# Kernel optimization log

Hardware: AMD Instinct MI355X
Metric: run time of the kernel (lower is better)

Reference implementation:

```python
import jax, jax.numpy as jnp
import numpy as np

N_NODES = 50000
N_EDGES = 640000
D_IN = 128
D_H = 128


def gcn_conv(x, edge_index_sl, W, b, n_nodes):
    # x: [N, d_in]; edge_index_sl: [2, E+N] (self-loops already appended)
    h = x @ W  # [N, d_out]
    row, col = edge_index_sl[0], edge_index_sl[1]
    deg = jax.ops.segment_sum(jnp.ones(row.shape[0], dtype=x.dtype), col,
                              num_segments=n_nodes)
    dis = jnp.where(deg > 0, jax.lax.rsqrt(jnp.maximum(deg, 1e-12)), 0.0)
    norm = dis[row] * dis[col]  # [E+N]
    msg = h[row] * norm[:, None]  # gather + scale, [E+N, d_out]
    out = jax.ops.segment_sum(msg, col, num_segments=n_nodes)  # scatter-add
    return out + b


def setup_inputs() -> dict:
    key = jax.random.key(0)
    ks = jax.random.split(key, 9)
    x = jax.random.normal(ks[0], (N_NODES, D_IN), dtype=jnp.float32)
    edge_index = jax.random.randint(ks[1], (2, N_EDGES), 0, N_NODES, dtype=jnp.int64)
    s0 = 1.0 / np.sqrt(D_IN)
    s1 = 1.0 / np.sqrt(D_H)
    W0 = jax.random.uniform(ks[2], (D_IN, D_H), jnp.float32, -s0, s0)
    b0 = jnp.zeros((D_H,), jnp.float32)
    W1 = jax.random.uniform(ks[3], (D_H, D_H), jnp.float32, -s1, s1)
    b1 = jnp.zeros((D_H,), jnp.float32)
    W2 = jax.random.uniform(ks[4], (D_H, D_H), jnp.float32, -s1, s1)
    b2 = jnp.zeros((D_H,), jnp.float32)
    return {"x": x, "edge_index": edge_index, "W0": W0, "b0": b0,
            "W1": W1, "b1": b1, "W2": W2, "b2": b2}


def reference(x, edge_index, W0, b0, W1, b1, W2, b2):
    n = x.shape[0]
    # GCNConv adds self-loops: append (i, i) for every node.
    loops = jnp.arange(n, dtype=edge_index.dtype)
    ei = jnp.concatenate([edge_index, jnp.stack([loops, loops])], axis=1)
    h = x
    for W, b in ((W0, b0), (W1, b1), (W2, b2)):
        h = gcn_conv(h, ei, W, b, n)
        h = jax.nn.relu(h)  # dropout is identity in eval mode
    return h
```

## Files before the change

### kernel.cpp

```cpp
#include <hip/hip_runtime.h>
#include <hip/hip_bf16.h>

#define D 128
#define CAP 64
typedef _Float16 f16;
typedef unsigned short u16;
typedef f16 f16x8 __attribute__((ext_vector_type(8)));
typedef f16 f16x4 __attribute__((ext_vector_type(4)));
typedef float f32x4 __attribute__((ext_vector_type(4)));



__global__ void scatter_cvt_kernel(const int* __restrict__ row, const int* __restrict__ col,
                                   int* __restrict__ fill, u16* __restrict__ ssrc, int E,
                                   const float* __restrict__ W0, const float* __restrict__ W1,
                                   const float* __restrict__ W2,
                                   const float* __restrict__ b0, const float* __restrict__ b1,
                                   const float* __restrict__ b2,
                                   f16* __restrict__ WT, float* __restrict__ bperm) {
    const int EB = (E + 255) >> 8;
    const int b = blockIdx.x;
    if (b < EB) {
        int i = b * 256 + threadIdx.x;
        if (i < E) {
            int d = col[i];
            int p = atomicAdd(&fill[d], 1);
            if (p < CAP) ssrc[(size_t)d * CAP + p] = (u16)row[i];
        }
    } else {
        int id = (b - EB) * 256 + threadIdx.x;
        if (id < 49152) {
            int l = id >> 14;
            int e = id & 16383;
            int j = e >> 7;
            int nn = e & 127;
            int k = (l == 0) ? j : ((j >> 3) + 16 * (j & 7));
            const float* W = (l == 0) ? W0 : (l == 1) ? W1 : W2;
            WT[(size_t)l * 16384 + nn * 128 + j] = (f16)W[k * 128 + nn];
        } else if (id < 49536) {
            int j = id - 49152;
            int l = j >> 7;
            int pos = j & 127;
            int c = 16 * (pos & 7) + (pos >> 3);
            const float* bb = (l == 0) ? b0 : (l == 1) ? b1 : b2;
            bperm[l * 128 + pos] = bb[c];
        }
    }
}


template <bool A_F32>
__global__ __launch_bounds__(256) void gemm_mfma(const void* __restrict__ Aptr,
                                                 const f16* __restrict__ WT,
                                                 const int* __restrict__ fill,
                                                 f16* __restrict__ H, int n) {
    __shared__ f16 sW[128 * 128];
    const int tid  = threadIdx.x;
    const int w    = tid >> 6, lane = tid & 63;
    const int q    = lane >> 4, c = lane & 15;
    const int row0 = blockIdx.x * 64;

    int arow = row0 + w * 16 + c;
    if (arow >= n) arow = n - 1;

    f16x8 afr[4];
    if (A_F32) {
        float4 x0[4], x1[4];
        #pragma unroll
        for (int t = 0; t < 4; ++t) {
            const float* src = (const float*)Aptr + (size_t)arow * D + (t * 4 + q) * 8;
            x0[t] = *(const float4*)src;
            x1[t] = *(const float4*)(src + 4);
        }
        #pragma unroll
        for (int t = 0; t < 4; ++t) {
            f16x8 h;
            h[0] = (f16)x0[t].x; h[1] = (f16)x0[t].y; h[2] = (f16)x0[t].z; h[3] = (f16)x0[t].w;
            h[4] = (f16)x1[t].x; h[5] = (f16)x1[t].y; h[6] = (f16)x1[t].z; h[7] = (f16)x1[t].w;
            afr[t] = h;
        }
    } else {
        #pragma unroll
        for (int t = 0; t < 4; ++t)
            afr[t] = *(const f16x8*)((const f16*)Aptr + (size_t)arow * D + (t * 4 + q) * 8);
    }

    #pragma unroll
    for (int i = 0; i < 8; ++i) {
        int f = i * 256 + tid;
        int r = f >> 4, b = f & 15;
        int u = (r << 4) | (b ^ (r & 15));
        *(f16x8*)&sW[u * 8] = *(const f16x8*)&WT[(size_t)r * D + b * 8];
    }
    __syncthreads();

    f32x4 acc[8];
    #pragma unroll
    for (int nt = 0; nt < 8; ++nt) acc[nt] = (f32x4)0.f;

    #pragma unroll
    for (int nt = 0; nt < 8; ++nt) {
        const int rn = nt * 16 + c;
        #pragma unroll
        for (int t = 0; t < 4; ++t) {
            f16x8 bfr = *(const f16x8*)&sW[(((rn << 4) | ((t * 4 + q) ^ c))) * 8];
            acc[nt] = __builtin_amdgcn_mfma_f32_16x16x32_f16(afr[t], bfr, acc[nt], 0, 0, 0);
        }
    }

    const int rbase = row0 + w * 16 + q * 4;
    int4 fv4 = *(const int4*)&fill[rbase];
    #pragma unroll
    for (int reg = 0; reg < 4; ++reg) {
        int grow = rbase + reg;
        if (grow < n) {
            int fv = (reg == 0) ? fv4.x : (reg == 1) ? fv4.y : (reg == 2) ? fv4.z : fv4.w;
            float dv = rsqrtf((float)(fv + 1));
            f16x8 hh;
            #pragma unroll
            for (int nt = 0; nt < 8; ++nt) hh[nt] = (f16)(acc[nt][reg] * dv);
            *(f16x8*)&H[(size_t)grow * D + c * 8] = hh;
        } else {
            const f16x8 z = {};
            *(f16x8*)&H[(size_t)grow * D + c * 8] = z;
        }
    }
}


template <bool LAST>
__global__ __launch_bounds__(256) void agg_kernel(const f16* __restrict__ H,
                                                  const int* __restrict__ fill,
                                                  const u16* __restrict__ ssrc,
                                                  const float* __restrict__ bperm,
                                                  float* __restrict__ out,
                                                  f16* __restrict__ act, int n) {
    const int tid  = threadIdx.x;
    const int wid  = (blockIdx.x << 2) | (tid >> 6);
    const int half = (tid >> 5) & 1;
    const int l    = tid & 31;
    int v = wid * 2 + half;
    const bool valid = (v < n);
    if (!valid) v = n - 1;
    const int fo = l * 4;
    const int zr = n;

    const u16* sp = &ssrc[(size_t)v * CAP];

    int4 sv0 = *(const int4*)sp;
    int4 sv1 = *(const int4*)(sp + 8);
    f16x4 hv = *(const f16x4*)&H[(size_t)v * D + fo];
    const int truedeg = fill[v];

    int deg = truedeg > CAP ? CAP : truedeg;
    int nb  = (deg + 15) >> 4;
    int nbo = __shfl_xor(nb, 32);
    const int nbmax = nb > nbo ? nb : nbo;

    float a0 = (float)hv[0], a1 = (float)hv[1], a2 = (float)hv[2], a3 = (float)hv[3];

    for (int b = 0; b < nbmax; ++b) {
        const int4 c0 = sv0, c1 = sv1;
        if (b + 1 < nbmax) {
            sv0 = *(const int4*)(sp + (b + 1) * 16);
            sv1 = *(const int4*)(sp + (b + 1) * 16 + 8);
        }
        const int rem = deg - b * 16;
        const int wv[8] = {c0.x, c0.y, c0.z, c0.w, c1.x, c1.y, c1.z, c1.w};
        f16x4 g[16];
        #pragma unroll
        for (int j = 0; j < 16; ++j) {
            int iv = (wv[j >> 1] >> ((j & 1) * 16)) & 0xffff;
            iv = (j < rem) ? iv : zr;
            g[j] = *(const f16x4*)&H[(size_t)iv * D + fo];
        }
        #pragma unroll
        for (int j = 0; j < 16; j += 4) {
            a0 += ((float)g[j][0] + (float)g[j + 1][0]) + ((float)g[j + 2][0] + (float)g[j + 3][0]);
            a1 += ((float)g[j][1] + (float)g[j + 1][1]) + ((float)g[j + 2][1] + (float)g[j + 3][1]);
            a2 += ((float)g[j][2] + (float)g[j + 1][2]) + ((float)g[j + 2][2] + (float)g[j + 3][2]);
            a3 += ((float)g[j][3] + (float)g[j + 1][3]) + ((float)g[j + 2][3] + (float)g[j + 3][3]);
        }
    }

    const float dv = rsqrtf((float)(truedeg + 1));
    const float4 bb = *(const float4*)&bperm[fo];
    float r0 = fmaxf(fmaf(dv, a0, bb.x), 0.f);
    float r1 = fmaxf(fmaf(dv, a1, bb.y), 0.f);
    float r2 = fmaxf(fmaf(dv, a2, bb.z), 0.f);
    float r3 = fmaxf(fmaf(dv, a3, bb.w), 0.f);

    if (valid) {
        if (LAST) {
            const int cb = (l & 1) * 64 + (l >> 1);
            float* op = out + (size_t)v * D + cb;
            op[0]  = r0;
            op[16] = r1;
            op[32] = r2;
            op[48] = r3;
        } else {
            f16x4 res;
            res[0] = (f16)r0; res[1] = (f16)r1; res[2] = (f16)r2; res[3] = (f16)r3;
            *(f16x4*)&act[(size_t)v * D + fo] = res;
        }
    }
}


extern "C" void kernel_launch(void* const* d_in, const int* in_sizes, int n_in,
                              void* d_out, int out_size, void* d_ws, size_t ws_size,
                              hipStream_t stream) {
    const float* x  = (const float*)d_in[0];
    const int*   ei = (const int*)d_in[1];
    const float* W0 = (const float*)d_in[2];
    const float* b0 = (const float*)d_in[3];
    const float* W1 = (const float*)d_in[4];
    const float* b1 = (const float*)d_in[5];
    const float* W2 = (const float*)d_in[6];
    const float* b2 = (const float*)d_in[7];
    float* out = (float*)d_out;

    const int n = in_sizes[0] / D;
    const int E = in_sizes[1] / 2;
    const int n_pad = (n + 64) & ~63;
    const int* row = ei;
    const int* col = ei + E;
    const int EB = (E + 255) / 256;

    char* w = (char*)d_ws;
    size_t o = 0;
    f16* hbuf = (f16*)(w + o); o += (size_t)n_pad * D * 2;
    f16* act  = (f16*)(w + o); o += (size_t)n_pad * D * 2;
    f16* WT   = (f16*)(w + o); o += (size_t)3 * 16384 * 2;
    o = (o + 63) & ~(size_t)63;
    float* bperm = (float*)(w + o); o += 3 * 128 * 4;
    int* fill = (int*)(w + o); o += (size_t)n_pad * 4;
    o = (o + 127) & ~(size_t)127;
    u16* ssrc = (u16*)(w + o);

    hipMemsetAsync(fill, 0, (size_t)n_pad * 4, stream);
    scatter_cvt_kernel<<<EB + 194, 256, 0, stream>>>(row, col, fill, ssrc, E,
                                                     W0, W1, W2, b0, b1, b2, WT, bperm);

    const int gblocks = n_pad >> 6;
    const int aggwaves = (n + 1) >> 1;
    const int ablocks = (aggwaves + 3) >> 2;

    gemm_mfma<true><<<gblocks, 256, 0, stream>>>(x, WT, fill, hbuf, n);
    agg_kernel<false><<<ablocks, 256, 0, stream>>>(hbuf, fill, ssrc, bperm, out, act, n);
    gemm_mfma<false><<<gblocks, 256, 0, stream>>>(act, WT + 16384, fill, hbuf, n);
    agg_kernel<false><<<ablocks, 256, 0, stream>>>(hbuf, fill, ssrc, bperm + 128, out, act, n);
    gemm_mfma<false><<<gblocks, 256, 0, stream>>>(act, WT + 2 * 16384, fill, hbuf, n);
    agg_kernel<true><<<ablocks, 256, 0, stream>>>(hbuf, fill, ssrc, bperm + 256, out, act, n);
}
```

Measured before the change: 235.3 us.

## Fuse aggregation with next layer's GEMM via shared-memory activation tile

The layer-1 and layer-2 aggregations are merged with the following layer's MFMA GEMM into one kernel. Each wave aggregates 16 rows into a swizzled LDS tile, then feeds that tile directly as the A fragment. This removes the f16 activation round trip through global memory and two kernel launches, and ping-pongs between two H buffers. In exchange each block reloads the 32KB weight tile and uses more LDS, which lowers occupancy for the latency-bound gather phase. Each wave also processes 8 node pairs serially, giving less parallelism per wave than the standalone aggregation kernel.

```diff
diff --git a/kernel.cpp b/kernel.cpp
--- a/kernel.cpp
+++ b/kernel.cpp
@@ -49,8 +49,7 @@
 }
 
 
-template <bool A_F32>
-__global__ __launch_bounds__(256) void gemm_mfma(const void* __restrict__ Aptr,
+__global__ __launch_bounds__(256) void gemm_mfma(const float* __restrict__ Aptr,
                                                  const f16* __restrict__ WT,
                                                  const int* __restrict__ fill,
                                                  f16* __restrict__ H, int n) {
@@ -64,11 +63,11 @@
     if (arow >= n) arow = n - 1;
 
     f16x8 afr[4];
-    if (A_F32) {
+    {
         float4 x0[4], x1[4];
         #pragma unroll
         for (int t = 0; t < 4; ++t) {
-            const float* src = (const float*)Aptr + (size_t)arow * D + (t * 4 + q) * 8;
+            const float* src = Aptr + (size_t)arow * D + (t * 4 + q) * 8;
             x0[t] = *(const float4*)src;
             x1[t] = *(const float4*)(src + 4);
         }
@@ -79,10 +78,6 @@
             h[4] = (f16)x1[t].x; h[5] = (f16)x1[t].y; h[6] = (f16)x1[t].z; h[7] = (f16)x1[t].w;
             afr[t] = h;
         }
-    } else {
-        #pragma unroll
-        for (int t = 0; t < 4; ++t)
-            afr[t] = *(const f16x8*)((const f16*)Aptr + (size_t)arow * D + (t * 4 + q) * 8);
     }
 
     #pragma unroll
@@ -128,13 +123,129 @@
 }
 
 
-template <bool LAST>
-__global__ __launch_bounds__(256) void agg_kernel(const f16* __restrict__ H,
-                                                  const int* __restrict__ fill,
-                                                  const u16* __restrict__ ssrc,
-                                                  const float* __restrict__ bperm,
-                                                  float* __restrict__ out,
-                                                  f16* __restrict__ act, int n) {
+__global__ __launch_bounds__(256) void fused_agg_gemm(const f16* __restrict__ Hin,
+                                                      const int* __restrict__ fill,
+                                                      const u16* __restrict__ ssrc,
+                                                      const float* __restrict__ bperm,
+                                                      const f16* __restrict__ WT,
+                                                      f16* __restrict__ Hout, int n) {
+    __shared__ f16 sW[128 * 128];
+    __shared__ f16 sA[4][16 * 128];
+    const int tid  = threadIdx.x;
+    const int w    = tid >> 6, lane = tid & 63;
+    const int q    = lane >> 4, c = lane & 15;
+    const int row0 = blockIdx.x * 64;
+
+    #pragma unroll
+    for (int i = 0; i < 8; ++i) {
+        int f = i * 256 + tid;
+        int r = f >> 4, b = f & 15;
+        int u = (r << 4) | (b ^ (r & 15));
+        *(f16x8*)&sW[u * 8] = *(const f16x8*)&WT[(size_t)r * D + b * 8];
+    }
+    __syncthreads();
+
+    const int h32 = (lane >> 5) & 1;
+    const int l   = lane & 31;
+    const int fo  = l * 4;
+    const int zr  = n;
+    const float4 bb = *(const float4*)&bperm[fo];
+
+    for (int p = 0; p < 8; ++p) {
+        int v = row0 + w * 16 + p * 2 + h32;
+        int vc = (v < n) ? v : (n - 1);
+        const u16* sp = &ssrc[(size_t)vc * CAP];
+        int4 sv0 = *(const int4*)sp;
+        int4 sv1 = *(const int4*)(sp + 8);
+        f16x4 hv = *(const f16x4*)&Hin[(size_t)vc * D + fo];
+        const int truedeg = fill[vc];
+
+        int deg = truedeg > CAP ? CAP : truedeg;
+        int nb  = (deg + 15) >> 4;
+        int nbo = __shfl_xor(nb, 32);
+        const int nbmax = nb > nbo ? nb : nbo;
+
+        float a0 = (float)hv[0], a1 = (float)hv[1], a2 = (float)hv[2], a3 = (float)hv[3];
+
+        for (int b = 0; b < nbmax; ++b) {
+            const int4 c0 = sv0, c1 = sv1;
+            if (b + 1 < nbmax) {
+                sv0 = *(const int4*)(sp + (b + 1) * 16);
+                sv1 = *(const int4*)(sp + (b + 1) * 16 + 8);
+            }
+            const int rem = deg - b * 16;
+            const int wv[8] = {c0.x, c0.y, c0.z, c0.w, c1.x, c1.y, c1.z, c1.w};
+            f16x4 g[16];
+            #pragma unroll
+            for (int j = 0; j < 16; ++j) {
+                int iv = (wv[j >> 1] >> ((j & 1) * 16)) & 0xffff;
+                iv = (j < rem) ? iv : zr;
+                g[j] = *(const f16x4*)&Hin[(size_t)iv * D + fo];
+            }
+            #pragma unroll
+            for (int j = 0; j < 16; j += 4) {
+                a0 += ((float)g[j][0] + (float)g[j+1][0]) + ((float)g[j+2][0] + (float)g[j+3][0]);
+                a1 += ((float)g[j][1] + (float)g[j+1][1]) + ((float)g[j+2][1] + (float)g[j+3][1]);
+                a2 += ((float)g[j][2] + (float)g[j+1][2]) + ((float)g[j+2][2] + (float)g[j+3][2]);
+                a3 += ((float)g[j][3] + (float)g[j+1][3]) + ((float)g[j+2][3] + (float)g[j+3][3]);
+            }
+        }
+
+        const float dv = rsqrtf((float)(truedeg + 1));
+        f16x4 res;
+        res[0] = (f16)fmaxf(fmaf(dv, a0, bb.x), 0.f);
+        res[1] = (f16)fmaxf(fmaf(dv, a1, bb.y), 0.f);
+        res[2] = (f16)fmaxf(fmaf(dv, a2, bb.z), 0.f);
+        res[3] = (f16)fmaxf(fmaf(dv, a3, bb.w), 0.f);
+
+        const int rL = p * 2 + h32;
+        *(f16x4*)&sA[w][((((rL << 4) | ((l >> 1) ^ (rL & 15)))) << 3) + (l & 1) * 4] = res;
+    }
+
+    f16x8 afr[4];
+    #pragma unroll
+    for (int t = 0; t < 4; ++t)
+        afr[t] = *(const f16x8*)&sA[w][(((c << 4) | ((t * 4 + q) ^ (c & 15)))) << 3];
+
+    f32x4 acc[8];
+    #pragma unroll
+    for (int nt = 0; nt < 8; ++nt) acc[nt] = (f32x4)0.f;
+
+    #pragma unroll
+    for (int nt = 0; nt < 8; ++nt) {
+        const int rn = nt * 16 + c;
+        #pragma unroll
+        for (int t = 0; t < 4; ++t) {
+            f16x8 bfr = *(const f16x8*)&sW[(((rn << 4) | ((t * 4 + q) ^ c))) * 8];
+            acc[nt] = __builtin_amdgcn_mfma_f32_16x16x32_f16(afr[t], bfr, acc[nt], 0, 0, 0);
+        }
+    }
+
+    const int rbase = row0 + w * 16 + q * 4;
+    int4 fv4 = *(const int4*)&fill[rbase];
+    #pragma unroll
+    for (int reg = 0; reg < 4; ++reg) {
+        int grow = rbase + reg;
+        if (grow < n) {
+            int fv = (reg == 0) ? fv4.x : (reg == 1) ? fv4.y : (reg == 2) ? fv4.z : fv4.w;
+            float dv = rsqrtf((float)(fv + 1));
+            f16x8 hh;
+            #pragma unroll
+            for (int nt = 0; nt < 8; ++nt) hh[nt] = (f16)(acc[nt][reg] * dv);
+            *(f16x8*)&Hout[(size_t)grow * D + c * 8] = hh;
+        } else {
+            const f16x8 z = {};
+            *(f16x8*)&Hout[(size_t)grow * D + c * 8] = z;
+        }
+    }
+}
+
+
+__global__ __launch_bounds__(256) void agg_last(const f16* __restrict__ H,
+                                                const int* __restrict__ fill,
+                                                const u16* __restrict__ ssrc,
+                                                const float* __restrict__ bperm,
+                                                float* __restrict__ out, int n) {
     const int tid  = threadIdx.x;
     const int wid  = (blockIdx.x << 2) | (tid >> 6);
     const int half = (tid >> 5) & 1;
@@ -146,7 +257,6 @@
     const int zr = n;
 
     const u16* sp = &ssrc[(size_t)v * CAP];
-
     int4 sv0 = *(const int4*)sp;
     int4 sv1 = *(const int4*)(sp + 8);
     f16x4 hv = *(const f16x4*)&H[(size_t)v * D + fo];
@@ -176,10 +286,10 @@
         }
         #pragma unroll
         for (int j = 0; j < 16; j += 4) {
-            a0 += ((float)g[j][0] + (float)g[j + 1][0]) + ((float)g[j + 2][0] + (float)g[j + 3][0]);
-            a1 += ((float)g[j][1] + (float)g[j + 1][1]) + ((float)g[j + 2][1] + (float)g[j + 3][1]);
-            a2 += ((float)g[j][2] + (float)g[j + 1][2]) + ((float)g[j + 2][2] + (float)g[j + 3][2]);
-            a3 += ((float)g[j][3] + (float)g[j + 1][3]) + ((float)g[j + 2][3] + (float)g[j + 3][3]);
+            a0 += ((float)g[j][0] + (float)g[j+1][0]) + ((float)g[j+2][0] + (float)g[j+3][0]);
+            a1 += ((float)g[j][1] + (float)g[j+1][1]) + ((float)g[j+2][1] + (float)g[j+3][1]);
+            a2 += ((float)g[j][2] + (float)g[j+1][2]) + ((float)g[j+2][2] + (float)g[j+3][2]);
+            a3 += ((float)g[j][3] + (float)g[j+1][3]) + ((float)g[j+2][3] + (float)g[j+3][3]);
         }
     }
 
@@ -191,18 +301,12 @@
     float r3 = fmaxf(fmaf(dv, a3, bb.w), 0.f);
 
     if (valid) {
-        if (LAST) {
-            const int cb = (l & 1) * 64 + (l >> 1);
-            float* op = out + (size_t)v * D + cb;
-            op[0]  = r0;
-            op[16] = r1;
-            op[32] = r2;
-            op[48] = r3;
-        } else {
-            f16x4 res;
-            res[0] = (f16)r0; res[1] = (f16)r1; res[2] = (f16)r2; res[3] = (f16)r3;
-            *(f16x4*)&act[(size_t)v * D + fo] = res;
-        }
+        const int cb = (l & 1) * 64 + (l >> 1);
+        float* op = out + (size_t)v * D + cb;
+        op[0]  = r0;
+        op[16] = r1;
+        op[32] = r2;
+        op[48] = r3;
     }
 }
 
@@ -229,9 +333,9 @@
 
     char* w = (char*)d_ws;
     size_t o = 0;
-    f16* hbuf = (f16*)(w + o); o += (size_t)n_pad * D * 2;
-    f16* act  = (f16*)(w + o); o += (size_t)n_pad * D * 2;
-    f16* WT   = (f16*)(w + o); o += (size_t)3 * 16384 * 2;
+    f16* hbufA = (f16*)(w + o); o += (size_t)n_pad * D * 2;
+    f16* hbufB = (f16*)(w + o); o += (size_t)n_pad * D * 2;
+    f16* WT    = (f16*)(w + o); o += (size_t)3 * 16384 * 2;
     o = (o + 63) & ~(size_t)63;
     float* bperm = (float*)(w + o); o += 3 * 128 * 4;
     int* fill = (int*)(w + o); o += (size_t)n_pad * 4;
@@ -246,10 +350,10 @@
     const int aggwaves = (n + 1) >> 1;
     const int ablocks = (aggwaves + 3) >> 2;
 
-    gemm_mfma<true><<<gblocks, 256, 0, stream>>>(x, WT, fill, hbuf, n);
-    agg_kernel<false><<<ablocks, 256, 0, stream>>>(hbuf, fill, ssrc, bperm, out, act, n);
-    gemm_mfma<false><<<gblocks, 256, 0, stream>>>(act, WT + 16384, fill, hbuf, n);
-    agg_kernel<false><<<ablocks, 256, 0, stream>>>(hbuf, fill, ssrc, bperm + 128, out, act, n);
-    gemm_mfma<false><<<gblocks, 256, 0, stream>>>(act, WT + 2 * 16384, fill, hbuf, n);
-    agg_kernel<true><<<ablocks, 256, 0, stream>>>(hbuf, fill, ssrc, bperm + 256, out, act, n);
-}
+    gemm_mfma<<<gblocks, 256, 0, stream>>>(x, WT, fill, hbufA, n);
+    fused_agg_gemm<<<gblocks, 256, 0, stream>>>(hbufA, fill, ssrc, bperm, WT + 16384,
+                                                hbufB, n);
+    fused_agg_gemm<<<gblocks, 256, 0, stream>>>(hbufB, fill, ssrc, bperm + 128,
+                                                WT + 2 * 16384, hbufA, n);
+    agg_last<<<ablocks, 256, 0, stream>>>(hbufA, fill, ssrc, bperm + 256, out, n);
+}
```

New measurement: 252.6 us. 7.3% more time.
